# Kernel tuning notes

Measured on AMD Instinct MI355X. Metric: run time of the kernel, lower is better.

The kernel has to match this reference:

```python
import jax, jax.numpy as jnp
import numpy as np

SCALES = (0, 1, 2, 3)
SIGMA_NSQ = 2.0
SIGMA_MAX_INV = 4.0 / (255.0 * 255.0)
GAIN_LIMIT = 100.0  # NEG=False
EPS = 1e-10


def gaussian_kernel_2d(N):
    sigma = N / 5.0
    x = jnp.arange(N, dtype=jnp.float32) - (N - 1) / 2.0
    g = jnp.exp(-(x * x) / (2.0 * sigma * sigma))
    k = jnp.outer(g, g)
    return (k / jnp.sum(k))[None, None]  # [1,1,N,N]


def reflect_pad(x, p):
    return jnp.pad(x, ((0, 0), (0, 0), (p, p), (p, p)), mode='reflect')


def conv2d(x, w, stride=1, groups=1):
    return jax.lax.conv_general_dilated(
        x, w, (stride, stride), 'VALID',
        dimension_numbers=('NCHW', 'OIHW', 'NCHW'),
        feature_group_count=groups)


def vif_num_den(ref, dist):
    ref = ref - 128.0
    dist = dist - 128.0
    h, w = ref.shape[-2], ref.shape[-1]
    nums, dens = [], []
    for scale in SCALES:
        N = 2 ** (4 - scale) + 1
        win = gaussian_kernel_2d(N)
        p = (N - 1) // 2
        if scale > 0:
            h, w = h // 2, w // 2
            ref = conv2d(reflect_pad(ref, p), win, stride=2)[:, :, :h, :w]
            dist = conv2d(reflect_pad(dist, p), win, stride=2)[:, :, :h, :w]
        win5 = jnp.tile(win, (5, 1, 1, 1))  # grouped conv, 5 channels
        inp = jnp.concatenate([ref, dist, ref * ref, dist * dist, ref * dist], axis=1)
        out = conv2d(reflect_pad(inp, p), win5, groups=5)  # [b,5,h,w]
        mu1, mu2, s1, s2, s12 = [out[:, i:i + 1] for i in range(5)]
        s1 = jax.nn.relu(s1 - mu1 * mu1)
        s2 = jax.nn.relu(s2 - mu2 * mu2)
        s12 = s12 - mu1 * mu2
        g = s12 / (s1 + EPS)
        sv = s2 - g * s12
        m1 = s1 < EPS
        g = jnp.where(m1, 0.0, g)
        sv = jnp.where(m1, s2, sv)
        s1 = jnp.where(m1, 0.0, s1)
        m2 = s2 < EPS
        g = jnp.where(m2, 0.0, g)
        sv = jnp.where(m2, 0.0, sv)
        sv = jnp.where(g < 0.0, s2, sv)
        g = jax.nn.relu(g)
        sv = jnp.where(sv <= EPS, EPS, sv)
        g = jnp.minimum(g, GAIN_LIMIT)
        num_ar = jnp.log2(1.0 + g * g * s1 / (sv + SIGMA_NSQ))
        den_ar = jnp.log2(1.0 + s1 / SIGMA_NSQ)
        num_ar = jnp.where(s12 < 0.0, 0.0, num_ar)
        m3 = s1 < SIGMA_NSQ
        num_ar = jnp.where(m3, 1.0 - s2 * SIGMA_MAX_INV, num_ar)
        den_ar = jnp.where(m3, 1.0, den_ar)
        nums.append(jnp.sum(num_ar, axis=(-1, -2, -3)))
        dens.append(jnp.sum(den_ar, axis=(-1, -2, -3)))
    return jnp.stack(nums, axis=-1), jnp.stack(dens, axis=-1)


def setup_inputs() -> dict:
    key = jax.random.key(0)
    k1, k2 = jax.random.split(key)
    shape = (4, 1, 1080, 1920)
    ref = jax.random.uniform(k1, shape, dtype=jnp.float32) * 255.0
    dist = jax.random.uniform(k2, shape, dtype=jnp.float32) * 255.0
    return {"ref": ref, "dist": dist}


def reference(ref, dist):
    num, den = vif_num_den(ref, dist)
    return num / den  # VIF features per scale, shape [b, 4]
```

## Files before the change

### kernel.cpp

```cpp
#include <hip/hip_runtime.h>
#include <math.h>

#define VIF_EPS       1e-10f
#define SIGMA_NSQ     2.0f
#define SIGMA_MAX_INV (4.0f / (255.0f * 255.0f))
#define GAIN_LIMIT    100.0f

typedef float v2f __attribute__((ext_vector_type(2)));
typedef float v4f __attribute__((ext_vector_type(4)));

static __device__ __forceinline__ v2f splat2(float s) {
    v2f v; v.x = s; v.y = s; return v;
}

__device__ __forceinline__ int reflect_idx(int i, int n) {
    i = (i < 0) ? -i : i;
    i = (i >= n) ? (2 * n - 2 - i) : i;
    return i;
}

template <int N>
__device__ __forceinline__ void fill_weights_global(float* gw) {
    const float sigma = (float)N / 5.0f;
    const float denom = 2.0f * sigma * sigma;
    float tmp[N];
    float s = 0.0f;
    for (int i = 0; i < N; ++i) {
        float x = (float)i - (float)(N - 1) * 0.5f;
        float g = expf(-(x * x) / denom);
        tmp[i] = g;
        s += g;
    }
    for (int i = 0; i < N; ++i) gw[i] = tmp[i] / s;
}

__global__ __launch_bounds__(64) void init_weights_kernel(float* __restrict__ gw) {
    const int tid = threadIdx.x;
    if (tid == 0) fill_weights_global<17>(gw + 0);
    else if (tid == 1) fill_weights_global<9>(gw + 17);
    else if (tid == 2) fill_weights_global<5>(gw + 26);
    else if (tid == 3) fill_weights_global<3>(gw + 31);
}

__host__ __device__ constexpr int w_off(int N) {
    return (N == 17) ? 0 : (N == 9) ? 17 : (N == 5) ? 26 : 31;
}

constexpr int tile_w(int N) { return (256 - (N - 1)) & ~3; }

template <int N>
struct alignas(16) StatsSmem {
    v2f   a[8][256];
    v2f   bq[8][256];
    float c[8][256];
};
template <int N>
struct alignas(16) DownSmem {
    v2f vb[8][252];
};

template <int N>
__device__ __forceinline__ void stats_body(
    StatsSmem<N>& sm, const float* __restrict__ refp, const float* __restrict__ distp,
    const float* __restrict__ gw,
    int h, int w, float shift, double2* __restrict__ partial,
    int sy, int sx, int bx, int b) {
    constexpr int P   = (N - 1) / 2;
    constexpr int TW  = tile_w(N);
    constexpr int TH  = 8;
    constexpr int LR  = TH + 2 * P;
    constexpr int XG4 = TW / 4;
    constexpr int NT  = TH * XG4;
    constexpr int REPS = (NT + 255) / 256;

    const int tid = threadIdx.x;
    const int ytile = bx % sy;
    const int xtile = bx / sy;
    const int x0 = xtile * TW;
    const int y0 = ytile * TH;

    float wr[N];
#pragma unroll
    for (int j = 0; j < N; ++j) wr[j] = gw[j];

    {
        const int cc = tid;
        const int gx = reflect_idx(x0 + cc - P, w);
        const float* rbase = refp  + (size_t)b * h * w;
        const float* dbase = distp + (size_t)b * h * w;

        v2f accA[TH], accB[TH];
        float accC[TH];
#pragma unroll
        for (int t = 0; t < TH; ++t) {
            accA[t] = splat2(0.f);
            accB[t] = splat2(0.f);
            accC[t] = 0.f;
        }

        auto acc_push = [&](int i, float r, float d) {
            v2f rd; rd.x = r; rd.y = d;
            v2f sq = rd * rd;
            float x = r * d;
#pragma unroll
            for (int t = 0; t < TH; ++t) {
                const int j = i - t;
                if (j >= 0 && j < N) {
                    const float wj = wr[j];
                    accA[t] += splat2(wj) * rd;
                    accB[t] += splat2(wj) * sq;
                    accC[t] += wj * x;
                }
            }
        };

        const int rowlo = y0 - P;
        if (rowlo >= 0 && rowlo + LR <= h) {
            unsigned voff = (unsigned)(rowlo * w + gx) * 4u;
            const unsigned vstep = (unsigned)w * 4u;
#pragma unroll
            for (int i = 0; i < LR; ++i) {
                float r = *(const float*)((const char*)rbase + voff) - shift;
                float d = *(const float*)((const char*)dbase + voff) - shift;
                voff += vstep;
                acc_push(i, r, d);
            }
        } else {
#pragma unroll
            for (int i = 0; i < LR; ++i) {
                const int gy = reflect_idx(rowlo + i, h);
                const size_t o = (size_t)gy * w + gx;
                float r = rbase[o] - shift;
                float d = dbase[o] - shift;
                acc_push(i, r, d);
            }
        }
#pragma unroll
        for (int t = 0; t < TH; ++t) {
            sm.a[t][cc]  = accA[t];
            sm.bq[t][cc] = accB[t];
            sm.c[t][cc]  = accC[t];
        }
    }
    __syncthreads();

    float num_v = 0.f, den_v = 0.f;
    {
        constexpr int WC  = N + 3;
        constexpr int F4C = (WC + 3) / 4;
#pragma unroll
        for (int rep = 0; rep < REPS; ++rep) {
            const int task = tid + 256 * rep;
            if (task < NT) {
                const int row = task / XG4;
                const int xg  = task - row * XG4;

                v2f muA[4], muB[4];
                float muC[4];
#pragma unroll
                for (int q = 0; q < 4; ++q) {
                    muA[q] = splat2(0.f);
                    muB[q] = splat2(0.f);
                    muC[q] = 0.f;
                }

                const v4f* A4 = (const v4f*)&sm.a[row][xg * 4];
                const v4f* B4 = (const v4f*)&sm.bq[row][xg * 4];
#pragma unroll
                for (int f = 0; f < WC / 2; ++f) {
                    v4f ta = A4[f];
                    v4f tb = B4[f];
#pragma unroll
                    for (int hlf = 0; hlf < 2; ++hlf) {
                        const int k = 2 * f + hlf;
                        v2f pa = hlf ? __builtin_shufflevector(ta, ta, 2, 3)
                                     : __builtin_shufflevector(ta, ta, 0, 1);
                        v2f pb = hlf ? __builtin_shufflevector(tb, tb, 2, 3)
                                     : __builtin_shufflevector(tb, tb, 0, 1);
#pragma unroll
                        for (int q = 0; q < 4; ++q) {
                            const int j = k - q;
                            if (j >= 0 && j < N) {
                                const float wj = wr[j];
                                muA[q] += splat2(wj) * pa;
                                muB[q] += splat2(wj) * pb;
                            }
                        }
                    }
                }
                {
                    const v4f* C4 = (const v4f*)&sm.c[row][xg * 4];
#pragma unroll
                    for (int f = 0; f < F4C; ++f) {
                        v4f t = C4[f];
#pragma unroll
                        for (int e = 0; e < 4; ++e) {
                            const int k = 4 * f + e;
                            const float x = (e == 0) ? t.x : (e == 1) ? t.y
                                          : (e == 2) ? t.z : t.w;
#pragma unroll
                            for (int q = 0; q < 4; ++q) {
                                const int j = k - q;
                                if (j >= 0 && j < N) muC[q] += wr[j] * x;
                            }
                        }
                    }
                }

                const int gy = y0 + row;
#pragma unroll
                for (int q = 0; q < 4; ++q) {
                    int gx = x0 + xg * 4 + q;
                    if (gx < w && gy < h) {
                        float mu1 = muA[q].x, mu2 = muA[q].y;
                        float s1  = fmaxf(0.f, muB[q].x - mu1 * mu1);
                        float s2  = fmaxf(0.f, muB[q].y - mu2 * mu2);
                        float s12 = muC[q] - mu1 * mu2;

                        float g  = s12 / (s1 + VIF_EPS);
                        float sv = s2 - g * s12;
                        if (s1 < VIF_EPS) { g = 0.f; sv = s2; s1 = 0.f; }
                        if (s2 < VIF_EPS) { g = 0.f; sv = 0.f; }
                        if (g  < 0.f)     { sv = s2; g = 0.f; }
                        if (sv <= VIF_EPS) sv = VIF_EPS;
                        g = fminf(g, GAIN_LIMIT);

                        float num_ar = __log2f(1.f + g * g * s1 / (sv + SIGMA_NSQ));
                        float den_ar = __log2f(1.f + s1 / SIGMA_NSQ);
                        if (s12 < 0.f) num_ar = 0.f;
                        if (s1 < SIGMA_NSQ) { num_ar = 1.f - s2 * SIGMA_MAX_INV; den_ar = 1.f; }
                        num_v += num_ar;
                        den_v += den_ar;
                    }
                }
            }
        }
    }

#pragma unroll
    for (int off = 32; off > 0; off >>= 1) {
        num_v += __shfl_down(num_v, off);
        den_v += __shfl_down(den_v, off);
    }
    __syncthreads();
    float* rs = reinterpret_cast<float*>(&sm);
    const int wid = tid >> 6, lane = tid & 63;
    if (lane == 0) { rs[wid] = num_v; rs[4 + wid] = den_v; }
    __syncthreads();
    if (tid == 0) {
        float ns = rs[0] + rs[1] + rs[2] + rs[3];
        float ds = rs[4] + rs[5] + rs[6] + rs[7];
        partial[(size_t)b * (sy * sx) + bx] = make_double2((double)ns, (double)ds);
    }
}

template <int N>
__device__ __forceinline__ void down_body(
    DownSmem<N>& sm, const float* __restrict__ rin, const float* __restrict__ din,
    const float* __restrict__ gw,
    float* __restrict__ rout, float* __restrict__ dout,
    int h, int w, int h2, int w2, float shift, int dgx, int bx, int b) {
    constexpr int P   = (N - 1) / 2;
    constexpr int TOW = 120, TOH = 8;
    constexpr int IC  = 2 * (TOW - 1) + N;
    constexpr int NR  = 2 * (TOH - 1) + N;
    constexpr int XG4 = TOW / 4;
    constexpr int WL  = N + 6;

    float wr[N];
#pragma unroll
    for (int j = 0; j < N; ++j) wr[j] = gw[j];

    const int tid = threadIdx.x;
    const int xt  = bx % dgx;
    const int yt  = bx / dgx;
    const int x0  = xt * TOW;
    const int y0  = yt * TOH;

    if (tid < IC) {
        const int gx = reflect_idx(2 * x0 - P + tid, w);
        const int rowlo = 2 * y0 - P;
        const float* rbase = rin + (size_t)b * h * w;
        const float* dbase = din + (size_t)b * h * w;

        v2f acc[TOH];
#pragma unroll
        for (int t = 0; t < TOH; ++t) acc[t] = splat2(0.f);

        const bool interior = (rowlo >= 0) && (rowlo + NR <= h);
        if (interior) {
            unsigned voff = (unsigned)(rowlo * w + gx) * 4u;
            const unsigned vstep = (unsigned)w * 4u;
#pragma unroll
            for (int i = 0; i < NR; ++i) {
                v2f x;
                x.x = *(const float*)((const char*)rbase + voff) - shift;
                x.y = *(const float*)((const char*)dbase + voff) - shift;
                voff += vstep;
#pragma unroll
                for (int t = 0; t < TOH; ++t) {
                    const int j = i - 2 * t;
                    if (j >= 0 && j < N) acc[t] += splat2(wr[j]) * x;
                }
            }
        } else {
#pragma unroll
            for (int i = 0; i < NR; ++i) {
                const int gy = reflect_idx(rowlo + i, h);
                const size_t o = (size_t)gy * w + gx;
                v2f x; x.x = rbase[o] - shift; x.y = dbase[o] - shift;
#pragma unroll
                for (int t = 0; t < TOH; ++t) {
                    const int j = i - 2 * t;
                    if (j >= 0 && j < N) acc[t] += splat2(wr[j]) * x;
                }
            }
        }
#pragma unroll
        for (int t = 0; t < TOH; ++t) sm.vb[t][tid] = acc[t];
    }
    __syncthreads();

    if (tid < TOH * XG4) {
        const int row = tid / XG4;
        const int xg  = tid - row * XG4;

        v2f o[4];
#pragma unroll
        for (int q = 0; q < 4; ++q) o[q] = splat2(0.f);

        const v4f* s4 = (const v4f*)&sm.vb[row][8 * xg];
#pragma unroll
        for (int f = 0; f < (WL + 1) / 2; ++f) {
            v4f t = s4[f];
#pragma unroll
            for (int hlf = 0; hlf < 2; ++hlf) {
                const int k = 2 * f + hlf;
                v2f p = hlf ? __builtin_shufflevector(t, t, 2, 3)
                            : __builtin_shufflevector(t, t, 0, 1);
#pragma unroll
                for (int q = 0; q < 4; ++q) {
                    const int j = k - 2 * q;
                    if (j >= 0 && j < N) o[q] += splat2(wr[j]) * p;
                }
            }
        }
        const int gy = y0 + row;
        if (gy < h2) {
            float* rp = rout + (size_t)b * h2 * w2 + (size_t)gy * w2 + x0 + 4 * xg;
            float* dp = dout + (size_t)b * h2 * w2 + (size_t)gy * w2 + x0 + 4 * xg;
            *(float4*)rp = make_float4(o[0].x, o[1].x, o[2].x, o[3].x);
            *(float4*)dp = make_float4(o[0].y, o[1].y, o[2].y, o[3].y);
        }
    }
}

template <int NS, int ND>
__global__ __launch_bounds__(256) void fused_kernel(
    const float* __restrict__ sref, const float* __restrict__ sdist,
    const float* __restrict__ gw,
    int sh, int sw, float sshift, double2* __restrict__ partial, int sy, int sx,
    float* __restrict__ drout, float* __restrict__ ddout,
    int dh2, int dw2, int dgx, int nStats) {
    __shared__ union {
        StatsSmem<NS> s;
        DownSmem<ND>  d;
    } u;
    const int bx = blockIdx.x;
    const int b  = blockIdx.z;
    if (bx < nStats)
        stats_body<NS>(u.s, sref, sdist, gw + w_off(NS), sh, sw, sshift,
                       partial, sy, sx, bx, b);
    else
        down_body<ND>(u.d, sref, sdist, gw + w_off(ND), drout, ddout,
                      sh, sw, dh2, dw2, sshift, dgx, bx - nStats, b);
}

template <int N>
__global__ __launch_bounds__(256) void stats_only_kernel(
    const float* __restrict__ refp, const float* __restrict__ distp,
    const float* __restrict__ gw,
    int h, int w, float shift, double2* __restrict__ partial, int sy, int sx) {
    __shared__ StatsSmem<N> sm;
    stats_body<N>(sm, refp, distp, gw + w_off(N), h, w, shift, partial,
                  sy, sx, blockIdx.x, blockIdx.z);
}

__global__ __launch_bounds__(256) void reduce_kernel(
    const double2* __restrict__ part, float* __restrict__ out,
    int4 bases, int4 counts) {
    __shared__ double sn[4], sd[4];
    const int s = blockIdx.x & 3;
    const int b = blockIdx.x >> 2;
    const int base = (&bases.x)[s];
    const int cnt  = (&counts.x)[s];
    const double2* p = part + base + (size_t)b * cnt;

    double ns = 0.0, ds = 0.0;
    for (int i = threadIdx.x; i < cnt; i += 256) {
        double2 v = p[i];
        ns += v.x;
        ds += v.y;
    }
#pragma unroll
    for (int off = 32; off > 0; off >>= 1) {
        ns += __shfl_down(ns, off);
        ds += __shfl_down(ds, off);
    }
    const int wid = threadIdx.x >> 6, lane = threadIdx.x & 63;
    if (lane == 0) { sn[wid] = ns; sd[wid] = ds; }
    __syncthreads();
    if (threadIdx.x == 0) {
        double Nv = sn[0] + sn[1] + sn[2] + sn[3];
        double Dv = sd[0] + sd[1] + sd[2] + sd[3];
        out[b * 4 + s] = (float)(Nv / Dv);
    }
}

extern "C" void kernel_launch(void* const* d_in, const int* in_sizes, int n_in,
                              void* d_out, int out_size, void* d_ws, size_t ws_size,
                              hipStream_t stream) {
    const float* ref  = (const float*)d_in[0];
    const float* dist = (const float*)d_in[1];
    float* out = (float*)d_out;

    const int B = 4;
    const int H0 = 1080, W0 = 1920;
    const int H1 = 540,  W1 = 960;
    const int H2 = 270,  W2 = 480;
    const int H3 = 135,  W3 = 240;

    char*  ws  = (char*)d_ws;
    size_t off = 0;
    auto alloc = [&](size_t bytes) -> void* {
        void* p = ws + off;
        off += (bytes + 255) & ~(size_t)255;
        return p;
    };
    float* gw    = (float*)alloc(34 * sizeof(float));
    float* ref1  = (float*)alloc((size_t)B * H1 * W1 * 4);
    float* dist1 = (float*)alloc((size_t)B * H1 * W1 * 4);
    float* ref2  = (float*)alloc((size_t)B * H2 * W2 * 4);
    float* dist2 = (float*)alloc((size_t)B * H2 * W2 * 4);
    float* ref3  = (float*)alloc((size_t)B * H3 * W3 * 4);
    float* dist3 = (float*)alloc((size_t)B * H3 * W3 * 4);

    const int sx0 = (W0 + tile_w(17) - 1) / tile_w(17), sy0 = (H0 + 7) / 8;
    const int sx1 = (W1 + tile_w(9)  - 1) / tile_w(9),  sy1 = (H1 + 7) / 8;
    const int sx2 = (W2 + tile_w(5)  - 1) / tile_w(5),  sy2 = (H2 + 7) / 8;
    const int sx3 = (W3 + tile_w(3)  - 1) / tile_w(3),  sy3 = (H3 + 7) / 8;
    const int n0 = sx0 * sy0, n1 = sx1 * sy1, n2 = sx2 * sy2, n3 = sx3 * sy3;

    const int dgx1 = W1 / 120, nD1 = dgx1 * ((H1 + 7) / 8);
    const int dgx2 = W2 / 120, nD2 = dgx2 * ((H2 + 7) / 8);
    const int dgx3 = W3 / 120, nD3 = dgx3 * ((H3 + 7) / 8);

    double2* part = (double2*)alloc((size_t)B * (n0 + n1 + n2 + n3) * sizeof(double2));
    double2* p0 = part;
    double2* p1 = p0 + (size_t)B * n0;
    double2* p2 = p1 + (size_t)B * n1;
    double2* p3 = p2 + (size_t)B * n2;

    dim3 blk(256);

    init_weights_kernel<<<1, 64, 0, stream>>>(gw);

    fused_kernel<17, 9><<<dim3(n0 + nD1, 1, B), blk, 0, stream>>>(
        ref, dist, gw, H0, W0, 128.0f, p0, sy0, sx0,
        ref1, dist1, H1, W1, dgx1, n0);

    fused_kernel<9, 5><<<dim3(n1 + nD2, 1, B), blk, 0, stream>>>(
        ref1, dist1, gw, H1, W1, 0.0f, p1, sy1, sx1,
        ref2, dist2, H2, W2, dgx2, n1);

    fused_kernel<5, 3><<<dim3(n2 + nD3, 1, B), blk, 0, stream>>>(
        ref2, dist2, gw, H2, W2, 0.0f, p2, sy2, sx2,
        ref3, dist3, H3, W3, dgx3, n2);

    stats_only_kernel<3><<<dim3(n3, 1, B), blk, 0, stream>>>(
        ref3, dist3, gw, H3, W3, 0.0f, p3, sy3, sx3);

    reduce_kernel<<<16, 256, 0, stream>>>(
        part, out,
        make_int4(0, B * n0, B * (n0 + n1), B * (n0 + n1 + n2)),
        make_int4(n0, n1, n2, n3));
}
```

Measured before the change: 172.7 us.

## Merge all VIF stages into one persistent cooperative kernel with grid syncs

```diff
diff --git a/kernel.cpp b/kernel.cpp
--- a/kernel.cpp
+++ b/kernel.cpp
@@ -1,5 +1,8 @@
 #include <hip/hip_runtime.h>
+#include <hip/hip_cooperative_groups.h>
 #include <math.h>
+
+namespace cg = cooperative_groups;
 
 #define VIF_EPS       1e-10f
 #define SIGMA_NSQ     2.0f
@@ -34,19 +37,22 @@
     for (int i = 0; i < N; ++i) gw[i] = tmp[i] / s;
 }
 
-__global__ __launch_bounds__(64) void init_weights_kernel(float* __restrict__ gw) {
-    const int tid = threadIdx.x;
-    if (tid == 0) fill_weights_global<17>(gw + 0);
-    else if (tid == 1) fill_weights_global<9>(gw + 17);
-    else if (tid == 2) fill_weights_global<5>(gw + 26);
-    else if (tid == 3) fill_weights_global<3>(gw + 31);
-}
-
-__host__ __device__ constexpr int w_off(int N) {
-    return (N == 17) ? 0 : (N == 9) ? 17 : (N == 5) ? 26 : 31;
-}
-
 constexpr int tile_w(int N) { return (256 - (N - 1)) & ~3; }
+
+constexpr int BATCH = 4;
+constexpr int H0 = 1080, W0 = 1920;
+constexpr int H1 = 540,  W1 = 960;
+constexpr int H2 = 270,  W2 = 480;
+constexpr int H3 = 135,  W3 = 240;
+
+constexpr int cdiv(int a, int b) { return (a + b - 1) / b; }
+constexpr int SX0 = cdiv(W0, tile_w(17)), SY0 = cdiv(H0, 8), N0 = SX0 * SY0;
+constexpr int SX1 = cdiv(W1, tile_w(9)),  SY1 = cdiv(H1, 8), N1 = SX1 * SY1;
+constexpr int SX2 = cdiv(W2, tile_w(5)),  SY2 = cdiv(H2, 8), N2 = SX2 * SY2;
+constexpr int SX3 = cdiv(W3, tile_w(3)),  SY3 = cdiv(H3, 8), N3 = SX3 * SY3;
+constexpr int DGX1 = W1 / 120, ND1 = DGX1 * cdiv(H1, 8);
+constexpr int DGX2 = W2 / 120, ND2 = DGX2 * cdiv(H2, 8);
+constexpr int DGX3 = W3 / 120, ND3 = DGX3 * cdiv(H3, 8);
 
 template <int N>
 struct alignas(16) StatsSmem {
@@ -252,6 +258,7 @@
         float ds = rs[4] + rs[5] + rs[6] + rs[7];
         partial[(size_t)b * (sy * sx) + bx] = make_double2((double)ns, (double)ds);
     }
+    __syncthreads();
 }
 
 template <int N>
@@ -353,67 +360,107 @@
             *(float4*)dp = make_float4(o[0].y, o[1].y, o[2].y, o[3].y);
         }
     }
-}
-
-template <int NS, int ND>
-__global__ __launch_bounds__(256) void fused_kernel(
-    const float* __restrict__ sref, const float* __restrict__ sdist,
-    const float* __restrict__ gw,
-    int sh, int sw, float sshift, double2* __restrict__ partial, int sy, int sx,
-    float* __restrict__ drout, float* __restrict__ ddout,
-    int dh2, int dw2, int dgx, int nStats) {
+    __syncthreads();
+}
+
+struct MegaParams {
+    const float* ref; const float* dist;
+    float* gw;
+    float* ref1; float* dist1; float* ref2; float* dist2; float* ref3; float* dist3;
+    double2 *p0, *p1, *p2, *p3;
+    float* out;
+};
+
+__global__ __launch_bounds__(256) void mega_kernel(MegaParams P) {
     __shared__ union {
-        StatsSmem<NS> s;
-        DownSmem<ND>  d;
+        StatsSmem<17> s17; StatsSmem<9> s9; StatsSmem<5> s5; StatsSmem<3> s3;
+        DownSmem<9> d9; DownSmem<5> d5; DownSmem<3> d3;
+        struct { double sn[4], sd[4]; } red;
     } u;
-    const int bx = blockIdx.x;
-    const int b  = blockIdx.z;
-    if (bx < nStats)
-        stats_body<NS>(u.s, sref, sdist, gw + w_off(NS), sh, sw, sshift,
-                       partial, sy, sx, bx, b);
-    else
-        down_body<ND>(u.d, sref, sdist, gw + w_off(ND), drout, ddout,
-                      sh, sw, dh2, dw2, sshift, dgx, bx - nStats, b);
-}
-
-template <int N>
-__global__ __launch_bounds__(256) void stats_only_kernel(
-    const float* __restrict__ refp, const float* __restrict__ distp,
-    const float* __restrict__ gw,
-    int h, int w, float shift, double2* __restrict__ partial, int sy, int sx) {
-    __shared__ StatsSmem<N> sm;
-    stats_body<N>(sm, refp, distp, gw + w_off(N), h, w, shift, partial,
-                  sy, sx, blockIdx.x, blockIdx.z);
-}
-
-__global__ __launch_bounds__(256) void reduce_kernel(
-    const double2* __restrict__ part, float* __restrict__ out,
-    int4 bases, int4 counts) {
-    __shared__ double sn[4], sd[4];
-    const int s = blockIdx.x & 3;
-    const int b = blockIdx.x >> 2;
-    const int base = (&bases.x)[s];
-    const int cnt  = (&counts.x)[s];
-    const double2* p = part + base + (size_t)b * cnt;
-
-    double ns = 0.0, ds = 0.0;
-    for (int i = threadIdx.x; i < cnt; i += 256) {
-        double2 v = p[i];
-        ns += v.x;
-        ds += v.y;
-    }
-#pragma unroll
-    for (int off = 32; off > 0; off >>= 1) {
-        ns += __shfl_down(ns, off);
-        ds += __shfl_down(ds, off);
-    }
-    const int wid = threadIdx.x >> 6, lane = threadIdx.x & 63;
-    if (lane == 0) { sn[wid] = ns; sd[wid] = ds; }
-    __syncthreads();
-    if (threadIdx.x == 0) {
-        double Nv = sn[0] + sn[1] + sn[2] + sn[3];
-        double Dv = sd[0] + sd[1] + sd[2] + sd[3];
-        out[b * 4 + s] = (float)(Nv / Dv);
+    cg::grid_group grid = cg::this_grid();
+    const int nb  = gridDim.x;
+    const int bid = blockIdx.x;
+    const int tid = threadIdx.x;
+
+    if (bid == 0) {
+        if (tid == 0)      fill_weights_global<17>(P.gw + 0);
+        else if (tid == 1) fill_weights_global<9>(P.gw + 17);
+        else if (tid == 2) fill_weights_global<5>(P.gw + 26);
+        else if (tid == 3) fill_weights_global<3>(P.gw + 31);
+        __threadfence();
+    }
+    grid.sync();
+
+    for (int v = bid; v < (N0 + ND1) * BATCH; v += nb) {
+        const int b = v / (N0 + ND1), bx = v % (N0 + ND1);
+        if (bx < N0)
+            stats_body<17>(u.s17, P.ref, P.dist, P.gw + 0, H0, W0, 128.f,
+                           P.p0, SY0, SX0, bx, b);
+        else
+            down_body<9>(u.d9, P.ref, P.dist, P.gw + 17, P.ref1, P.dist1,
+                         H0, W0, H1, W1, 128.f, DGX1, bx - N0, b);
+    }
+    grid.sync();
+
+    for (int v = bid; v < (N1 + ND2) * BATCH; v += nb) {
+        const int b = v / (N1 + ND2), bx = v % (N1 + ND2);
+        if (bx < N1)
+            stats_body<9>(u.s9, P.ref1, P.dist1, P.gw + 17, H1, W1, 0.f,
+                          P.p1, SY1, SX1, bx, b);
+        else
+            down_body<5>(u.d5, P.ref1, P.dist1, P.gw + 26, P.ref2, P.dist2,
+                         H1, W1, H2, W2, 0.f, DGX2, bx - N1, b);
+    }
+    grid.sync();
+
+    for (int v = bid; v < (N2 + ND3) * BATCH; v += nb) {
+        const int b = v / (N2 + ND3), bx = v % (N2 + ND3);
+        if (bx < N2)
+            stats_body<5>(u.s5, P.ref2, P.dist2, P.gw + 26, H2, W2, 0.f,
+                          P.p2, SY2, SX2, bx, b);
+        else
+            down_body<3>(u.d3, P.ref2, P.dist2, P.gw + 31, P.ref3, P.dist3,
+                         H2, W2, H3, W3, 0.f, DGX3, bx - N2, b);
+    }
+    grid.sync();
+
+    for (int v = bid; v < N3 * BATCH; v += nb) {
+        const int b = v / N3, bx = v % N3;
+        stats_body<3>(u.s3, P.ref3, P.dist3, P.gw + 31, H3, W3, 0.f,
+                      P.p3, SY3, SX3, bx, b);
+    }
+    grid.sync();
+
+    for (int v = bid; v < 4 * BATCH; v += nb) {
+        const int s = v & 3;
+        const int b = v >> 2;
+        const double2* p; int cnt;
+        if (s == 0)      { p = P.p0; cnt = N0; }
+        else if (s == 1) { p = P.p1; cnt = N1; }
+        else if (s == 2) { p = P.p2; cnt = N2; }
+        else             { p = P.p3; cnt = N3; }
+        p += (size_t)b * cnt;
+
+        double ns = 0.0, ds = 0.0;
+        for (int i = tid; i < cnt; i += 256) {
+            double2 t = p[i];
+            ns += t.x;
+            ds += t.y;
+        }
+#pragma unroll
+        for (int off = 32; off > 0; off >>= 1) {
+            ns += __shfl_down(ns, off);
+            ds += __shfl_down(ds, off);
+        }
+        const int wid = tid >> 6, lane = tid & 63;
+        if (lane == 0) { u.red.sn[wid] = ns; u.red.sd[wid] = ds; }
+        __syncthreads();
+        if (tid == 0) {
+            double Nv = u.red.sn[0] + u.red.sn[1] + u.red.sn[2] + u.red.sn[3];
+            double Dv = u.red.sd[0] + u.red.sd[1] + u.red.sd[2] + u.red.sd[3];
+            P.out[b * 4 + s] = (float)(Nv / Dv);
+        }
+        __syncthreads();
     }
 }
 
@@ -423,12 +470,6 @@
     const float* ref  = (const float*)d_in[0];
     const float* dist = (const float*)d_in[1];
     float* out = (float*)d_out;
-
-    const int B = 4;
-    const int H0 = 1080, W0 = 1920;
-    const int H1 = 540,  W1 = 960;
-    const int H2 = 270,  W2 = 480;
-    const int H3 = 135,  W3 = 240;
 
     char*  ws  = (char*)d_ws;
     size_t off = 0;
@@ -438,50 +479,37 @@
         return p;
     };
     float* gw    = (float*)alloc(34 * sizeof(float));
-    float* ref1  = (float*)alloc((size_t)B * H1 * W1 * 4);
-    float* dist1 = (float*)alloc((size_t)B * H1 * W1 * 4);
-    float* ref2  = (float*)alloc((size_t)B * H2 * W2 * 4);
-    float* dist2 = (float*)alloc((size_t)B * H2 * W2 * 4);
-    float* ref3  = (float*)alloc((size_t)B * H3 * W3 * 4);
-    float* dist3 = (float*)alloc((size_t)B * H3 * W3 * 4);
-
-    const int sx0 = (W0 + tile_w(17) - 1) / tile_w(17), sy0 = (H0 + 7) / 8;
-    const int sx1 = (W1 + tile_w(9)  - 1) / tile_w(9),  sy1 = (H1 + 7) / 8;
-    const int sx2 = (W2 + tile_w(5)  - 1) / tile_w(5),  sy2 = (H2 + 7) / 8;
-    const int sx3 = (W3 + tile_w(3)  - 1) / tile_w(3),  sy3 = (H3 + 7) / 8;
-    const int n0 = sx0 * sy0, n1 = sx1 * sy1, n2 = sx2 * sy2, n3 = sx3 * sy3;
-
-    const int dgx1 = W1 / 120, nD1 = dgx1 * ((H1 + 7) / 8);
-    const int dgx2 = W2 / 120, nD2 = dgx2 * ((H2 + 7) / 8);
-    const int dgx3 = W3 / 120, nD3 = dgx3 * ((H3 + 7) / 8);
-
-    double2* part = (double2*)alloc((size_t)B * (n0 + n1 + n2 + n3) * sizeof(double2));
+    float* ref1  = (float*)alloc((size_t)BATCH * H1 * W1 * 4);
+    float* dist1 = (float*)alloc((size_t)BATCH * H1 * W1 * 4);
+    float* ref2  = (float*)alloc((size_t)BATCH * H2 * W2 * 4);
+    float* dist2 = (float*)alloc((size_t)BATCH * H2 * W2 * 4);
+    float* ref3  = (float*)alloc((size_t)BATCH * H3 * W3 * 4);
+    float* dist3 = (float*)alloc((size_t)BATCH * H3 * W3 * 4);
+
+    double2* part = (double2*)alloc((size_t)BATCH * (N0 + N1 + N2 + N3) * sizeof(double2));
     double2* p0 = part;
-    double2* p1 = p0 + (size_t)B * n0;
-    double2* p2 = p1 + (size_t)B * n1;
-    double2* p3 = p2 + (size_t)B * n2;
-
-    dim3 blk(256);
-
-    init_weights_kernel<<<1, 64, 0, stream>>>(gw);
-
-    fused_kernel<17, 9><<<dim3(n0 + nD1, 1, B), blk, 0, stream>>>(
-        ref, dist, gw, H0, W0, 128.0f, p0, sy0, sx0,
-        ref1, dist1, H1, W1, dgx1, n0);
-
-    fused_kernel<9, 5><<<dim3(n1 + nD2, 1, B), blk, 0, stream>>>(
-        ref1, dist1, gw, H1, W1, 0.0f, p1, sy1, sx1,
-        ref2, dist2, H2, W2, dgx2, n1);
-
-    fused_kernel<5, 3><<<dim3(n2 + nD3, 1, B), blk, 0, stream>>>(
-        ref2, dist2, gw, H2, W2, 0.0f, p2, sy2, sx2,
-        ref3, dist3, H3, W3, dgx3, n2);
-
-    stats_only_kernel<3><<<dim3(n3, 1, B), blk, 0, stream>>>(
-        ref3, dist3, gw, H3, W3, 0.0f, p3, sy3, sx3);
-
-    reduce_kernel<<<16, 256, 0, stream>>>(
-        part, out,
-        make_int4(0, B * n0, B * (n0 + n1), B * (n0 + n1 + n2)),
-        make_int4(n0, n1, n2, n3));
-}
+    double2* p1 = p0 + (size_t)BATCH * N0;
+    double2* p2 = p1 + (size_t)BATCH * N1;
+    double2* p3 = p2 + (size_t)BATCH * N2;
+
+    static int NB = 0;
+    if (NB <= 0) {
+        int maxB = 0;
+        if (hipOccupancyMaxActiveBlocksPerMultiprocessor(&maxB, mega_kernel, 256, 0)
+                != hipSuccess || maxB < 1)
+            maxB = 4;
+        NB = maxB * 256;
+        if (NB > (N0 + ND1) * BATCH) NB = (N0 + ND1) * BATCH;
+    }
+
+    MegaParams P;
+    P.ref = ref;   P.dist = dist;  P.gw = gw;
+    P.ref1 = ref1; P.dist1 = dist1;
+    P.ref2 = ref2; P.dist2 = dist2;
+    P.ref3 = ref3; P.dist3 = dist3;
+    P.p0 = p0; P.p1 = p1; P.p2 = p2; P.p3 = p3;
+    P.out = out;
+
+    void* kargs[] = { &P };
+    hipLaunchCooperativeKernel(mega_kernel, dim3(NB), dim3(256), kargs, 0, stream);
+}
```

Result: slower. 401.4 us (+132.4%).
